# Performance work log

Hardware: AMD Instinct MI355X
Metric: run time of the kernel (lower is better)

The kernel has to match this reference:

```python
import jax, jax.numpy as jnp
import numpy as np

N_NODES, N_EDGES, D_IN, D_HID, D_OUT = 100000, 3200000, 512, 64, 64


def _gcn_conv(x, W, b, src, dst, n_nodes):
    """PyG-style GCNConv: x' = D^{-1/2} A_hat D^{-1/2} (x W) + b, self-loops already in (src,dst)."""
    h = x @ W  # [N, F_out]
    deg = jax.ops.segment_sum(jnp.ones_like(dst, dtype=h.dtype), dst, num_segments=n_nodes)
    dinv = jax.lax.rsqrt(deg)  # deg >= 1 because self-loops are included
    norm = dinv[src] * dinv[dst]  # [E]
    msg = h[src] * norm[:, None]  # gather + scale, [E, F_out]
    return jax.ops.segment_sum(msg, dst, num_segments=n_nodes) + b


def setup_inputs() -> dict:
    key = jax.random.key(0)
    ks = jax.random.split(key, 8)
    x = jax.random.normal(ks[0], (N_NODES, D_IN), dtype=jnp.float32)
    edge_index = jax.random.randint(ks[1], (2, N_EDGES), 0, N_NODES, dtype=jnp.int32)
    W1 = jax.random.normal(ks[2], (D_IN, D_HID), dtype=jnp.float32) * (1.0 / np.sqrt(D_IN))
    b1 = jnp.zeros((D_HID,), dtype=jnp.float32)
    W2 = jax.random.normal(ks[3], (D_HID, D_OUT), dtype=jnp.float32) * (1.0 / np.sqrt(D_HID))
    b2 = jnp.zeros((D_OUT,), dtype=jnp.float32)
    Wlin = jax.random.normal(ks[4], (D_HID, D_OUT), dtype=jnp.float32) * (1.0 / np.sqrt(D_HID))
    blin = jnp.zeros((D_OUT,), dtype=jnp.float32)
    return {"x": x, "edge_index": edge_index, "W1": W1, "b1": b1,
            "W2": W2, "b2": b2, "Wlin": Wlin, "blin": blin}


def reference(x, edge_index, W1, b1, W2, b2, Wlin, blin):
    n = x.shape[0]
    loops = jnp.arange(n, dtype=edge_index.dtype)
    src = jnp.concatenate([edge_index[0], loops])
    dst = jnp.concatenate([edge_index[1], loops])
    h = _gcn_conv(x, W1, b1, src, dst, n)
    h = jax.nn.relu(h)
    h = _gcn_conv(h, W2, b2, src, dst, n)
    return h @ Wlin + blin
```

## Files before the change

### kernel.cpp

```cpp
#include <hip/hip_runtime.h>

#define DIN 512
#define DH  64
#define BKT_SHIFT 10
#define BKT_NODES 1024
#define MAXBKT 128
#define TILE 8192
#define SRC_BITS 17
#define SRC_MASK ((1u << SRC_BITS) - 1)

typedef __attribute__((ext_vector_type(8))) _Float16 half8_t;
typedef __attribute__((ext_vector_type(4))) float float4_t;

__global__ __launch_bounds__(256) void k_prepbin(const float* __restrict__ W1,
                                                 const float* __restrict__ W2,
                                                 const float* __restrict__ b2,
                                                 const float* __restrict__ Wlin,
                                                 const float* __restrict__ blin,
                                                 _Float16* __restrict__ Wt,
                                                 _Float16* __restrict__ Wct,
                                                 float* __restrict__ bias_out,
                                                 const int* __restrict__ src,
                                                 const int* __restrict__ dst,
                                                 int n_edges,
                                                 int* __restrict__ gcur,
                                                 unsigned int* __restrict__ tmp,
                                                 int nbkt, int cap) {
  const int tid = threadIdx.x;
  if (blockIdx.x == 0) {
    __shared__ float WcS[64 * 64];
    for (int idx = tid; idx < 64 * 64; idx += 256) {
      int i = idx >> 6, j = idx & 63;
      float s = 0.f;
      #pragma unroll 8
      for (int k = 0; k < 64; ++k) s = fmaf(W2[i * 64 + k], Wlin[k * 64 + j], s);
      WcS[idx] = s;
    }
    if (tid < 64) {
      float s = blin[tid];
      #pragma unroll 8
      for (int k = 0; k < 64; ++k) s = fmaf(b2[k], Wlin[k * 64 + tid], s);
      bias_out[tid] = s;
    }
    __syncthreads();
    for (int G = tid; G < 64 * 64 / 8; G += 256) {
      int n = G >> 3, k = (G & 7) * 8;
      half8_t h;
      #pragma unroll
      for (int j = 0; j < 8; ++j) h[j] = (_Float16)WcS[(k + j) * 64 + n];
      *(half8_t*)&Wct[(size_t)n * 64 + k] = h;
    }
  } else if (blockIdx.x <= 4) {
    __shared__ _Float16 T[64][136];
    const int k0 = (blockIdx.x - 1) * 128;
    for (int idx = tid; idx < 128 * 64; idx += 256) {
      int kk = idx >> 6, n = idx & 63;
      T[n][kk] = (_Float16)W1[(size_t)(k0 + kk) * 64 + n];
    }
    __syncthreads();
    for (int G = tid; G < 64 * 16; G += 256) {
      int n = G >> 4, g = (G & 15) * 8;
      half8_t h = *(const half8_t*)&T[n][g];
      *(half8_t*)&Wt[(size_t)n * 512 + k0 + g] = h;
    }
  } else {
    __shared__ int cnt[MAXBKT];
    __shared__ int base[MAXBKT];
    for (int b = tid; b < nbkt; b += 256) cnt[b] = 0;
    __syncthreads();
    int e0 = (blockIdx.x - 5) * TILE;
    int e1 = min(e0 + TILE, n_edges);
    for (int e = e0 + tid; e < e1; e += 256)
      atomicAdd(&cnt[dst[e] >> BKT_SHIFT], 1);
    __syncthreads();
    for (int b = tid; b < nbkt; b += 256) {
      int c = cnt[b];
      base[b] = c ? (b * cap + atomicAdd(&gcur[b], c)) : 0;
      cnt[b] = 0;
    }
    __syncthreads();
    for (int e = e0 + tid; e < e1; e += 256) {
      int d = dst[e];
      int bkt = d >> BKT_SHIFT;
      int off = atomicAdd(&cnt[bkt], 1);
      int pos = base[bkt] + off;
      if (pos < (bkt + 1) * cap)
        tmp[pos] = (unsigned int)src[e] |
                   ((unsigned int)(d & (BKT_NODES - 1)) << SRC_BITS);
    }
  }
}

__global__ __launch_bounds__(256) void k_place(const unsigned int* __restrict__ tmp,
                                               const int* __restrict__ gcur,
                                               int* __restrict__ rowbeg,
                                               int* __restrict__ rowcnt,
                                               float* __restrict__ dinv,
                                               int* __restrict__ srcs,
                                               int n_nodes, int cap) {
  __shared__ int cnt[BKT_NODES];
  __shared__ int sh[256];
  const int t = threadIdx.x;
  const int bkt = blockIdx.x;
  #pragma unroll
  for (int k = 0; k < BKT_NODES / 256; ++k) cnt[t + 256 * k] = 0;
  __syncthreads();
  const int beg = bkt * cap;
  const int end = beg + min(gcur[bkt], cap);
  for (int j = beg + t; j < end; j += 256)
    atomicAdd(&cnt[tmp[j] >> SRC_BITS], 1);
  __syncthreads();
  int v[4];
  int s = 0;
  const int base = t * 4;
  #pragma unroll
  for (int k = 0; k < 4; ++k) {
    v[k] = cnt[base + k];
    s += v[k];
  }
  sh[t] = s;
  __syncthreads();
  for (int off = 1; off < 256; off <<= 1) {
    int x = sh[t];
    int y = (t >= off) ? sh[t - off] : 0;
    __syncthreads();
    sh[t] = x + y;
    __syncthreads();
  }
  int excl = sh[t] - s;
  #pragma unroll
  for (int k = 0; k < 4; ++k) {
    int idx = base + k;
    int node = (bkt << BKT_SHIFT) + idx;
    if (node < n_nodes) {
      rowbeg[node] = beg + excl;
      rowcnt[node] = v[k];
      dinv[node] = rsqrtf((float)(v[k] + 1));
    }
    cnt[idx] = excl;
    excl += v[k];
  }
  __syncthreads();
  for (int j = beg + t; j < end; j += 256) {
    unsigned int e = tmp[j];
    int r = e >> SRC_BITS;
    int pos = atomicAdd(&cnt[r], 1);
    srcs[beg + pos] = (int)(e & SRC_MASK);
  }
}

template <int KDIM, bool A_HALF>
__global__ __launch_bounds__(1024) void k_mfma(const void* __restrict__ Ain,
                                               const _Float16* __restrict__ Bt,
                                               const float* __restrict__ dinv,
                                               _Float16* __restrict__ Ch, int M) {
  constexpr int BS_HALVES = (64 * KDIM > 16384) ? 64 * KDIM : 16384;
  __shared__ _Float16 Bs[BS_HALVES];
  const int tid = threadIdx.x;
  for (int G = tid; G < 8 * KDIM; G += 1024) {
    int n = G / (KDIM / 8);
    int g = G % (KDIM / 8);
    half8_t h = *(const half8_t*)&Bt[(size_t)G * 8];
    *(half8_t*)&Bs[n * KDIM + ((g ^ (n & 7)) * 8)] = h;
  }
  __syncthreads();

  const int wave = tid >> 6, lane = tid & 63;
  const int quad = lane >> 4, lrow = lane & 15;
  const int row = blockIdx.x * 256 + wave * 16 + lrow;
  const int rowc = min(row, M - 1);

  float4_t acc[4] = {{0.f, 0.f, 0.f, 0.f}, {0.f, 0.f, 0.f, 0.f},
                     {0.f, 0.f, 0.f, 0.f}, {0.f, 0.f, 0.f, 0.f}};

  #pragma unroll
  for (int k0 = 0; k0 < KDIM; k0 += 32) {
    half8_t a;
    if (A_HALF) {
      a = *(const half8_t*)((const _Float16*)Ain + (size_t)rowc * KDIM + k0 + quad * 8);
    } else {
      const float* Af = (const float*)Ain + (size_t)rowc * KDIM + k0 + quad * 8;
      float4 x0 = *(const float4*)Af;
      float4 x1 = *(const float4*)(Af + 4);
      a[0] = (_Float16)x0.x; a[1] = (_Float16)x0.y;
      a[2] = (_Float16)x0.z; a[3] = (_Float16)x0.w;
      a[4] = (_Float16)x1.x; a[5] = (_Float16)x1.y;
      a[6] = (_Float16)x1.z; a[7] = (_Float16)x1.w;
    }
    const int g = (k0 >> 3) + quad;
    #pragma unroll
    for (int nb = 0; nb < 4; ++nb) {
      int n = nb * 16 + lrow;
      half8_t b = *(const half8_t*)&Bs[n * KDIM + ((g ^ (n & 7)) * 8)];
      acc[nb] = __builtin_amdgcn_mfma_f32_16x16x32_f16(a, b, acc[nb], 0, 0, 0);
    }
  }

  const int orow_base = blockIdx.x * 256 + wave * 16 + quad * 4;
  float dnr[4];
  #pragma unroll
  for (int r = 0; r < 4; ++r) dnr[r] = dinv[min(orow_base + r, M - 1)];

  __syncthreads();
  _Float16* scratch = Bs + wave * 1024;
  #pragma unroll
  for (int nb = 0; nb < 4; ++nb)
    #pragma unroll
    for (int r = 0; r < 4; ++r)
      scratch[(quad * 4 + r) * 64 + nb * 16 + lrow] = (_Float16)(acc[nb][r] * dnr[r]);
  const int r2 = lane >> 2, c2 = (lane & 3) * 16;
  const int row_out = blockIdx.x * 256 + wave * 16 + r2;
  half8_t o0 = *(const half8_t*)&scratch[r2 * 64 + c2];
  half8_t o1 = *(const half8_t*)&scratch[r2 * 64 + c2 + 8];
  if (row_out < M) {
    *(half8_t*)&Ch[(size_t)row_out * 64 + c2] = o0;
    *(half8_t*)&Ch[(size_t)row_out * 64 + c2 + 8] = o1;
  }
}

__global__ __launch_bounds__(256) void k_gather(const _Float16* __restrict__ fs,
                                                const int* __restrict__ rowbeg,
                                                const int* __restrict__ rowcnt,
                                                const int* __restrict__ srcs,
                                                const float* __restrict__ dinv,
                                                const float* __restrict__ bias,
                                                _Float16* __restrict__ outh,
                                                float* __restrict__ outf,
                                                int n_nodes) {
  int node = __builtin_amdgcn_readfirstlane(blockIdx.x * 4 + (threadIdx.x >> 6));
  int lane = threadIdx.x & 63;
  if (node >= n_nodes) return;
  const int esub = lane >> 3;
  const int ch8 = (lane & 7) * 8;
  const int beg = rowbeg[node];
  const int end = beg + rowcnt[node];
  float acc[8] = {0.f, 0.f, 0.f, 0.f, 0.f, 0.f, 0.f, 0.f};
  int j = beg;
  for (; j + 32 <= end; j += 32) {
    int s0 = srcs[j + esub];
    int s1 = srcs[j + 8 + esub];
    int s2 = srcs[j + 16 + esub];
    int s3 = srcs[j + 24 + esub];
    half8_t f0 = *(const half8_t*)&fs[(size_t)s0 * 64 + ch8];
    half8_t f1 = *(const half8_t*)&fs[(size_t)s1 * 64 + ch8];
    half8_t f2 = *(const half8_t*)&fs[(size_t)s2 * 64 + ch8];
    half8_t f3 = *(const half8_t*)&fs[(size_t)s3 * 64 + ch8];
    #pragma unroll
    for (int k = 0; k < 8; ++k) acc[k] += (float)f0[k];
    #pragma unroll
    for (int k = 0; k < 8; ++k) acc[k] += (float)f1[k];
    #pragma unroll
    for (int k = 0; k < 8; ++k) acc[k] += (float)f2[k];
    #pragma unroll
    for (int k = 0; k < 8; ++k) acc[k] += (float)f3[k];
  }
  if (j + 16 <= end) {
    int s0 = srcs[j + esub];
    int s1 = srcs[j + 8 + esub];
    half8_t f0 = *(const half8_t*)&fs[(size_t)s0 * 64 + ch8];
    half8_t f1 = *(const half8_t*)&fs[(size_t)s1 * 64 + ch8];
    #pragma unroll
    for (int k = 0; k < 8; ++k) acc[k] += (float)f0[k];
    #pragma unroll
    for (int k = 0; k < 8; ++k) acc[k] += (float)f1[k];
    j += 16;
  }
  for (; j < end; j += 8) {
    int idx = j + esub;
    bool act = idx < end;
    int s = srcs[act ? idx : beg];
    float w = act ? 1.f : 0.f;
    half8_t f = *(const half8_t*)&fs[(size_t)s * 64 + ch8];
    #pragma unroll
    for (int k = 0; k < 8; ++k) acc[k] = fmaf((float)f[k], w, acc[k]);
  }
  #pragma unroll
  for (int m = 8; m <= 32; m <<= 1)
    #pragma unroll
    for (int k = 0; k < 8; ++k) acc[k] += __shfl_xor(acc[k], m, 64);
  if (esub == 0) {
    float dn = dinv[node];
    half8_t sf = *(const half8_t*)&fs[(size_t)node * 64 + ch8];
    float v[8];
    #pragma unroll
    for (int k = 0; k < 8; ++k)
      v[k] = fmaf(acc[k] + (float)sf[k], dn, bias[ch8 + k]);
    if (outh) {
      half8_t o;
      #pragma unroll
      for (int k = 0; k < 8; ++k) o[k] = (_Float16)fmaxf(v[k], 0.f);
      *(half8_t*)&outh[(size_t)node * 64 + ch8] = o;
    } else {
      float4 o0 = make_float4(v[0], v[1], v[2], v[3]);
      float4 o1 = make_float4(v[4], v[5], v[6], v[7]);
      *(float4*)&outf[(size_t)node * 64 + ch8] = o0;
      *(float4*)&outf[(size_t)node * 64 + ch8 + 4] = o1;
    }
  }
}

extern "C" void kernel_launch(void* const* d_in, const int* in_sizes, int n_in,
                              void* d_out, int out_size, void* d_ws, size_t ws_size,
                              hipStream_t stream) {
  const float* x    = (const float*)d_in[0];
  const int*   ei   = (const int*)d_in[1];
  const float* W1   = (const float*)d_in[2];
  const float* b1   = (const float*)d_in[3];
  const float* W2   = (const float*)d_in[4];
  const float* b2   = (const float*)d_in[5];
  const float* Wlin = (const float*)d_in[6];
  const float* blin = (const float*)d_in[7];
  float* out = (float*)d_out;

  const int n_nodes = in_sizes[0] / DIN;
  const int n_edges = in_sizes[1] / 2;
  const int* src = ei;
  const int* dst = ei + n_edges;
  const int nbkt = (n_nodes + BKT_NODES - 1) >> BKT_SHIFT;
  const int ntiles = (n_edges + TILE - 1) / TILE;
  const int cap = ((n_edges / nbkt) * 5 / 4 + 1024 + 255) & ~255;

  char* ws = (char*)d_ws;
  size_t off = 0;
  auto alloc = [&](size_t bytes) {
    void* p = ws + off;
    off += (bytes + 255) & ~(size_t)255;
    return p;
  };
  const size_t featH = (size_t)n_nodes * DH * 2;
  const size_t padE = (size_t)nbkt * cap;
  _Float16*     fs1      = (_Float16*)alloc(featH);
  _Float16*     h1r      = (_Float16*)alloc(featH);
  _Float16*     fs2      = (_Float16*)alloc(featH);
  unsigned int* tmp      = (unsigned int*)alloc(padE * 4);
  int*          srcs     = (int*)alloc(padE * 4);
  float*        dinv     = (float*)alloc((size_t)n_nodes * 4);
  int*          rowbeg   = (int*)alloc((size_t)n_nodes * 4);
  int*          rowcnt   = (int*)alloc((size_t)n_nodes * 4);
  int*          gcur     = (int*)alloc((size_t)MAXBKT * 4);
  _Float16*     Wt       = (_Float16*)alloc(64 * 512 * 2);
  _Float16*     Wct      = (_Float16*)alloc(64 * 64 * 2);
  float*        bias_out = (float*)alloc(64 * 4);

  hipMemsetAsync(gcur, 0, (size_t)nbkt * 4, stream);

  k_prepbin<<<5 + ntiles, 256, 0, stream>>>(W1, W2, b2, Wlin, blin, Wt, Wct,
                                            bias_out, src, dst, n_edges, gcur,
                                            tmp, nbkt, cap);
  k_place<<<nbkt, 256, 0, stream>>>(tmp, gcur, rowbeg, rowcnt, dinv, srcs,
                                    n_nodes, cap);

  const int mblocks = (n_nodes + 255) / 256;
  const int agblocks = (n_nodes + 3) / 4;

  k_mfma<512, false><<<mblocks, 1024, 0, stream>>>(x, Wt, dinv, fs1, n_nodes);
  k_gather<<<agblocks, 256, 0, stream>>>(fs1, rowbeg, rowcnt, srcs, dinv, b1,
                                         h1r, nullptr, n_nodes);

  k_mfma<64, true><<<mblocks, 1024, 0, stream>>>(h1r, Wct, dinv, fs2, n_nodes);
  k_gather<<<agblocks, 256, 0, stream>>>(fs2, rowbeg, rowcnt, srcs, dinv,
                                         bias_out, nullptr, out, n_nodes);
}
```

Measured before the change: 561.6 us.

## Cache dst in LDS, pack row metadata, hoist gather loads, nontemporal hints

The binning kernel now stages each tile's dst values in shared memory so the second pass does not re-read dst from global memory. Both src and dst are read with nontemporal loads. Row begin and count are packed into one int2 array, so the gather kernel does a single metadata load. The gather kernel also issues its dinv, self-feature and bias loads before the edge loop so their latency overlaps the gathers, and uses nontemporal loads for the edge index stream. The 32KB LDS buffer may lower occupancy of the binning blocks, and the hoisted values use more registers.

```diff
diff --git a/kernel.cpp b/kernel.cpp
--- a/kernel.cpp
+++ b/kernel.cpp
@@ -64,14 +64,18 @@
       *(half8_t*)&Wt[(size_t)n * 512 + k0 + g] = h;
     }
   } else {
+    __shared__ int dstS[TILE];
     __shared__ int cnt[MAXBKT];
     __shared__ int base[MAXBKT];
     for (int b = tid; b < nbkt; b += 256) cnt[b] = 0;
     __syncthreads();
     int e0 = (blockIdx.x - 5) * TILE;
     int e1 = min(e0 + TILE, n_edges);
-    for (int e = e0 + tid; e < e1; e += 256)
-      atomicAdd(&cnt[dst[e] >> BKT_SHIFT], 1);
+    for (int e = e0 + tid; e < e1; e += 256) {
+      int d = __builtin_nontemporal_load(&dst[e]);
+      dstS[e - e0] = d;
+      atomicAdd(&cnt[d >> BKT_SHIFT], 1);
+    }
     __syncthreads();
     for (int b = tid; b < nbkt; b += 256) {
       int c = cnt[b];
@@ -80,12 +84,12 @@
     }
     __syncthreads();
     for (int e = e0 + tid; e < e1; e += 256) {
-      int d = dst[e];
+      int d = dstS[e - e0];
       int bkt = d >> BKT_SHIFT;
       int off = atomicAdd(&cnt[bkt], 1);
       int pos = base[bkt] + off;
       if (pos < (bkt + 1) * cap)
-        tmp[pos] = (unsigned int)src[e] |
+        tmp[pos] = (unsigned int)__builtin_nontemporal_load(&src[e]) |
                    ((unsigned int)(d & (BKT_NODES - 1)) << SRC_BITS);
     }
   }
@@ -93,8 +97,7 @@
 
 __global__ __launch_bounds__(256) void k_place(const unsigned int* __restrict__ tmp,
                                                const int* __restrict__ gcur,
-                                               int* __restrict__ rowbeg,
-                                               int* __restrict__ rowcnt,
+                                               int2* __restrict__ rowmeta,
                                                float* __restrict__ dinv,
                                                int* __restrict__ srcs,
                                                int n_nodes, int cap) {
@@ -133,8 +136,7 @@
     int idx = base + k;
     int node = (bkt << BKT_SHIFT) + idx;
     if (node < n_nodes) {
-      rowbeg[node] = beg + excl;
-      rowcnt[node] = v[k];
+      rowmeta[node] = make_int2(beg + excl, v[k]);
       dinv[node] = rsqrtf((float)(v[k] + 1));
     }
     cnt[idx] = excl;
@@ -219,8 +221,7 @@
 }
 
 __global__ __launch_bounds__(256) void k_gather(const _Float16* __restrict__ fs,
-                                                const int* __restrict__ rowbeg,
-                                                const int* __restrict__ rowcnt,
+                                                const int2* __restrict__ rowmeta,
                                                 const int* __restrict__ srcs,
                                                 const float* __restrict__ dinv,
                                                 const float* __restrict__ bias,
@@ -232,15 +233,20 @@
   if (node >= n_nodes) return;
   const int esub = lane >> 3;
   const int ch8 = (lane & 7) * 8;
-  const int beg = rowbeg[node];
-  const int end = beg + rowcnt[node];
+  const int2 meta = rowmeta[node];
+  const int beg = meta.x;
+  const int end = beg + meta.y;
+  const float dn = dinv[node];
+  const half8_t sf = *(const half8_t*)&fs[(size_t)node * 64 + ch8];
+  const float4 bs0 = *(const float4*)&bias[ch8];
+  const float4 bs1 = *(const float4*)&bias[ch8 + 4];
   float acc[8] = {0.f, 0.f, 0.f, 0.f, 0.f, 0.f, 0.f, 0.f};
   int j = beg;
   for (; j + 32 <= end; j += 32) {
-    int s0 = srcs[j + esub];
-    int s1 = srcs[j + 8 + esub];
-    int s2 = srcs[j + 16 + esub];
-    int s3 = srcs[j + 24 + esub];
+    int s0 = __builtin_nontemporal_load(&srcs[j + esub]);
+    int s1 = __builtin_nontemporal_load(&srcs[j + 8 + esub]);
+    int s2 = __builtin_nontemporal_load(&srcs[j + 16 + esub]);
+    int s3 = __builtin_nontemporal_load(&srcs[j + 24 + esub]);
     half8_t f0 = *(const half8_t*)&fs[(size_t)s0 * 64 + ch8];
     half8_t f1 = *(const half8_t*)&fs[(size_t)s1 * 64 + ch8];
     half8_t f2 = *(const half8_t*)&fs[(size_t)s2 * 64 + ch8];
@@ -255,8 +261,8 @@
     for (int k = 0; k < 8; ++k) acc[k] += (float)f3[k];
   }
   if (j + 16 <= end) {
-    int s0 = srcs[j + esub];
-    int s1 = srcs[j + 8 + esub];
+    int s0 = __builtin_nontemporal_load(&srcs[j + esub]);
+    int s1 = __builtin_nontemporal_load(&srcs[j + 8 + esub]);
     half8_t f0 = *(const half8_t*)&fs[(size_t)s0 * 64 + ch8];
     half8_t f1 = *(const half8_t*)&fs[(size_t)s1 * 64 + ch8];
     #pragma unroll
@@ -279,12 +285,11 @@
     #pragma unroll
     for (int k = 0; k < 8; ++k) acc[k] += __shfl_xor(acc[k], m, 64);
   if (esub == 0) {
-    float dn = dinv[node];
-    half8_t sf = *(const half8_t*)&fs[(size_t)node * 64 + ch8];
+    float bsv[8] = {bs0.x, bs0.y, bs0.z, bs0.w, bs1.x, bs1.y, bs1.z, bs1.w};
     float v[8];
     #pragma unroll
     for (int k = 0; k < 8; ++k)
-      v[k] = fmaf(acc[k] + (float)sf[k], dn, bias[ch8 + k]);
+      v[k] = fmaf(acc[k] + (float)sf[k], dn, bsv[k]);
     if (outh) {
       half8_t o;
       #pragma unroll
@@ -335,8 +340,7 @@
   unsigned int* tmp      = (unsigned int*)alloc(padE * 4);
   int*          srcs     = (int*)alloc(padE * 4);
   float*        dinv     = (float*)alloc((size_t)n_nodes * 4);
-  int*          rowbeg   = (int*)alloc((size_t)n_nodes * 4);
-  int*          rowcnt   = (int*)alloc((size_t)n_nodes * 4);
+  int2*         rowmeta  = (int2*)alloc((size_t)n_nodes * 8);
   int*          gcur     = (int*)alloc((size_t)MAXBKT * 4);
   _Float16*     Wt       = (_Float16*)alloc(64 * 512 * 2);
   _Float16*     Wct      = (_Float16*)alloc(64 * 64 * 2);
@@ -347,17 +351,17 @@
   k_prepbin<<<5 + ntiles, 256, 0, stream>>>(W1, W2, b2, Wlin, blin, Wt, Wct,
                                             bias_out, src, dst, n_edges, gcur,
                                             tmp, nbkt, cap);
-  k_place<<<nbkt, 256, 0, stream>>>(tmp, gcur, rowbeg, rowcnt, dinv, srcs,
+  k_place<<<nbkt, 256, 0, stream>>>(tmp, gcur, rowmeta, dinv, srcs,
                                     n_nodes, cap);
 
   const int mblocks = (n_nodes + 255) / 256;
   const int agblocks = (n_nodes + 3) / 4;
 
   k_mfma<512, false><<<mblocks, 1024, 0, stream>>>(x, Wt, dinv, fs1, n_nodes);
-  k_gather<<<agblocks, 256, 0, stream>>>(fs1, rowbeg, rowcnt, srcs, dinv, b1,
+  k_gather<<<agblocks, 256, 0, stream>>>(fs1, rowmeta, srcs, dinv, b1,
                                          h1r, nullptr, n_nodes);
 
   k_mfma<64, true><<<mblocks, 1024, 0, stream>>>(h1r, Wct, dinv, fs2, n_nodes);
-  k_gather<<<agblocks, 256, 0, stream>>>(fs2, rowbeg, rowcnt, srcs, dinv,
+  k_gather<<<agblocks, 256, 0, stream>>>(fs2, rowmeta, srcs, dinv,
                                          bias_out, nullptr, out, n_nodes);
 }
```

Result: no change. 559.2 us (-0.4%).
